# Kernel tuning notes

Hardware: AMD Instinct MI355X
Metric: run time of the kernel (lower is better)

The kernel has to match this reference:

```python
import jax, jax.numpy as jnp
import numpy as np

MAX_REL = 30
N_HEADS = 8


def conv1d(x, w, b=None, groups=1):
    # x: [B, L, Cin], w: [Cout, Cin/groups, K]  (torch Conv1d layout), 'same' padding
    pad = w.shape[-1] // 2
    y = jax.lax.conv_general_dilated(
        x, w, window_strides=(1,), padding=[(pad, pad)],
        dimension_numbers=("NLC", "OIL", "NLC"), feature_group_count=groups)
    return y if b is None else y + b


def setup_inputs() -> dict:
    key = jax.random.key(0)
    ks = jax.random.split(key, 16)
    B, L, S = 8, 1024, 512          # L = 2 * S (required by Gamma.repeat(1,2,1))
    sd, vd, dm = 512, 64, 512       # spatial_dim == d_model (residual add)
    D = 3 * vd                      # rel-pos / K,V channel dim

    def n(k, shape, s):
        return (jax.random.normal(k, shape, jnp.float32) * s).astype(jnp.float32)

    return {
        "x_spatial": jax.random.normal(ks[0], (B, L, sd), jnp.float32),
        "x_velocity": jax.random.normal(ks[1], (B, S, vd), jnp.float32),
        "w_gamma": n(ks[2], (dm, vd, 1), 0.05)[:, :, 0],      # conv_gamma 1x1, no bias -> [dm, vd]
        "w3": n(ks[3], (vd, vd, 3), 0.07), "b3": jnp.zeros((vd,), jnp.float32),
        "w5": n(ks[4], (vd, vd, 5), 0.05), "b5": jnp.zeros((vd,), jnp.float32),
        "w7": n(ks[5], (vd, vd, 7), 0.04), "b7": jnp.zeros((vd,), jnp.float32),
        "rel_table": n(ks[6], (2 * MAX_REL + 1, D), 0.05),    # embedding [61, 192]
        "dw_w": n(ks[7], (D, 1, 3), 0.3), "dw_b": jnp.zeros((D,), jnp.float32),
        "wq": n(ks[8], (dm, sd), 0.03),
        "wk": n(ks[9], (dm, D), 0.05),
        "wv": n(ks[10], (dm, D), 0.05),
        "fc_w": n(ks[11], (dm, dm), 0.03), "fc_b": jnp.zeros((dm,), jnp.float32),
        "ln_g": jnp.ones((dm,), jnp.float32), "ln_b": jnp.zeros((dm,), jnp.float32),
    }


def rel_pos_enc(ms, rel_table, dw_w, dw_b):
    # Math-equivalent reduction of the torch O(B*S^2*D) op:
    # output[b,j] = mean_i where(i==j, dwconv_row_i(fused)[j], fused[b,i,j])
    #            = ms[b,j] + mean_i rel[i,j] + (diag_conv[b,j] - fused[b,j,j]) / S
    B, S, D = ms.shape
    pos = jnp.arange(S)
    idx = jnp.clip(pos[None, :] - pos[:, None], -MAX_REL, MAX_REL) + MAX_REL  # [S,S]
    mean_rel = rel_table[idx].mean(axis=0)                                    # [S,D]
    # fused[b,i,j] = ms[b,j] + rel_table[idx[i,j]]; diagonal uses idx = MAX_REL,
    # its +/-1 neighbors along j use MAX_REL -/+ ... -> rel[i,i-1]=MAX_REL-1, rel[i,i+1]=MAX_REL+1
    center = ms + rel_table[MAX_REL]                                          # fused[b,i,i]
    left = jnp.pad(ms[:, :-1] + rel_table[MAX_REL - 1], ((0, 0), (1, 0), (0, 0)))   # conv zero-pads at i=0
    right = jnp.pad(ms[:, 1:] + rel_table[MAX_REL + 1], ((0, 0), (0, 1), (0, 0)))   # conv zero-pads at i=S-1
    diag_conv = dw_w[:, 0, 0] * left + dw_w[:, 0, 1] * center + dw_w[:, 0, 2] * right + dw_b
    return ms + mean_rel[None] + (diag_conv - center) / S


def reference(x_spatial, x_velocity, w_gamma, w3, b3, w5, b5, w7, b7,
              rel_table, dw_w, dw_b, wq, wk, wv, fc_w, fc_b, ln_g, ln_b):
    B, S, vd = x_velocity.shape
    _, L, _ = x_spatial.shape
    dm = wq.shape[0]
    dk = dm // N_HEADS

    gamma = jax.nn.sigmoid(jnp.einsum("bsc,dc->bsd", x_velocity, w_gamma))   # [B,S,dm]

    ms = jnp.concatenate([conv1d(x_velocity, w3, b3),
                          conv1d(x_velocity, w5, b5),
                          conv1d(x_velocity, w7, b7)], axis=-1)              # [B,S,3vd]
    x_pe = rel_pos_enc(ms, rel_table, dw_w, dw_b)                            # [B,S,3vd]

    q = jnp.einsum("blc,dc->bld", x_spatial, wq).reshape(B, L, N_HEADS, dk).transpose(0, 2, 1, 3)
    k = jnp.einsum("bsc,dc->bsd", x_pe, wk).reshape(B, S, N_HEADS, dk).transpose(0, 2, 1, 3)
    v = jnp.einsum("bsc,dc->bsd", x_pe, wv).reshape(B, S, N_HEADS, dk).transpose(0, 2, 1, 3)

    scores = jnp.einsum("bhld,bhsd->bhls", q, k) / jnp.sqrt(jnp.float32(dk))
    attn = jax.nn.softmax(scores, axis=-1)                                   # dropout: eval mode (identity)
    out = jnp.einsum("bhls,bhsd->bhld", attn, v)                             # [B,H,L,dk]
    out = out.transpose(0, 2, 1, 3).reshape(B, L, dm)
    out = out @ fc_w.T + fc_b

    out = jnp.tile(gamma, (1, 2, 1)) * out                                   # L == 2*S
    res = x_spatial + out
    mu = res.mean(-1, keepdims=True)
    var = res.var(-1, keepdims=True)
    return (res - mu) / jnp.sqrt(var + 1e-5) * ln_g + ln_b
```

## Files before the change

### kernel.cpp

```cpp
#include <hip/hip_runtime.h>
#include <hip/hip_bf16.h>

constexpr int B  = 8;
constexpr int L  = 1024;
constexpr int S  = 512;
constexpr int VD = 64;
constexpr int DM = 512;
constexpr int D3 = 192;
constexpr int H  = 8;
constexpr int DK = 64;

typedef __attribute__((ext_vector_type(8))) short s8v;
typedef __attribute__((ext_vector_type(4))) float f4v;

__device__ inline unsigned short f2b(float f) {
    unsigned int u = __builtin_bit_cast(unsigned int, f);
    u += 0x7fffu + ((u >> 16) & 1u);
    return (unsigned short)(u >> 16);
}
__device__ inline float b2f(unsigned int lo16) {
    return __builtin_bit_cast(float, lo16 << 16);
}

__device__ __forceinline__ void gload16(const void* g, void* l) {
    __builtin_amdgcn_global_load_lds(
        (const __attribute__((address_space(1))) void*)g,
        (__attribute__((address_space(3))) void*)l, 16, 0, 0);
}

struct CastArgs {
    const float* src[7];
    unsigned short* dst[7];
    int n[7];
    float scale[7];
};

__global__ __launch_bounds__(256) void prep_cast_k(
    CastArgs a,
    const float* __restrict__ w3, const float* __restrict__ w5,
    const float* __restrict__ w7, const float* __restrict__ dw_w,
    const float* __restrict__ rel_table, const float* __restrict__ b3,
    const float* __restrict__ b5, const float* __restrict__ b7,
    const float* __restrict__ dw_b,
    unsigned short* __restrict__ WpeT, unsigned short* __restrict__ Cp)
{
    int t = threadIdx.x;
    int y = blockIdx.y;

    if (y < 7) {
        const float* s = a.src[y];
        unsigned short* d = a.dst[y];
        int n = a.n[y];
        float sc = a.scale[y];
        for (long i = (long)(blockIdx.x * 256 + t) * 4; i < n;
             i += (long)gridDim.x * 1024) {
            float4 f = *(const float4*)(s + i);
            ushort4 o;
            o.x = f2b(f.x * sc); o.y = f2b(f.y * sc);
            o.z = f2b(f.z * sc); o.w = f2b(f.w * sc);
            *(ushort4*)(d + i) = o;
        }
        return;
    }

    if (t >= 192) return;
    int o = t;
    float inv = 1.0f / S;

    if (blockIdx.x < 640) {
        int n = blockIdx.x;
        if (n >= 576) { WpeT[n * D3 + o] = 0; return; }
        int j = n >> 6, c = n & 63, delta = j - 4;
        const float* w; int KW, P, oo;
        if (o < 64)       { w = w3; KW = 3; P = 1; oo = o; }
        else if (o < 128) { w = w5; KW = 5; P = 2; oo = o - 64; }
        else              { w = w7; KW = 7; P = 3; oo = o - 128; }
        float mu0 = dw_w[o * 3 + 0] * inv;
        float mu1 = 1.f + (dw_w[o * 3 + 1] - 1.f) * inv;
        float mu2 = dw_w[o * 3 + 2] * inv;
        float acc = 0.f;
        int k;
        k = delta + 1 + P; if (k >= 0 && k < KW) acc += mu0 * w[(oo * 64 + c) * KW + k];
        k = delta + P;     if (k >= 0 && k < KW) acc += mu1 * w[(oo * 64 + c) * KW + k];
        k = delta - 1 + P; if (k >= 0 && k < KW) acc += mu2 * w[(oo * 64 + c) * KW + k];
        WpeT[n * D3 + o] = f2b(acc);
        return;
    }

    int j = blockIdx.x - 640;
    float acc = 0.f;
#pragma unroll
    for (int r = 1; r < 60; r++) {
        int i = j - (r - 30);
        if (i >= 0 && i < S) acc += rel_table[r * D3 + o];
    }
    float c60 = (float)max(0, j - 29);
    float c0  = (float)max(0, (S - 30) - j);
    acc += c60 * rel_table[60 * D3 + o] + c0 * rel_table[0 * D3 + o];
    float mean_rel = acc * inv;

    float bo  = (o < 64) ? b3[o] : (o < 128) ? b5[o - 64] : b7[o - 128];
    float dw0 = dw_w[o * 3], dw1 = dw_w[o * 3 + 1], dw2 = dw_w[o * 3 + 2];
    float r29 = rel_table[29 * D3 + o], r30 = rel_table[30 * D3 + o],
          r31 = rel_table[31 * D3 + o];
    float alpha = 1.f + (dw1 - 1.f) * inv, beta = dw0 * inv, gamma = dw2 * inv;

    float cp = mean_rel + bo * alpha + (dw1 * r30 + dw_b[o] - r30) * inv;
    if (j > 0)     cp += beta * bo + dw0 * r29 * inv;
    if (j < S - 1) cp += gamma * bo + dw2 * r31 * inv;
    Cp[j * D3 + o] = f2b(cp);
}

__global__ __launch_bounds__(256) void pre_gemm5_k(
    const unsigned short* __restrict__ wk_bf,
    const unsigned short* __restrict__ wv_bf,
    const unsigned short* __restrict__ WpeT,
    const unsigned short* __restrict__ Cp,
    const unsigned short* __restrict__ xv_bf,
    const unsigned short* __restrict__ wg_bf,
    unsigned short* __restrict__ WEff,
    unsigned short* __restrict__ Cb,
    unsigned short* __restrict__ gamma_bf)
{
    int z = blockIdx.z, mx = blockIdx.x, ny = blockIdx.y;
    const unsigned short *A, *Bm;
    unsigned short* C;
    int K, lda, ldb, ldc;
    if (z < 2) {
        if (mx >= 4) return;
        A = z ? wv_bf : wk_bf; Bm = WpeT; C = WEff + (long)z * DM * 640;
        K = D3; lda = D3; ldb = D3; ldc = 640;
    } else if (z < 4) {
        if (mx >= 4 || ny >= 4) return;
        A = Cp; Bm = (z == 2) ? wk_bf : wv_bf; C = Cb + (long)(z - 2) * S * DM;
        K = D3; lda = D3; ldb = D3; ldc = DM;
    } else {
        if (ny >= 4) return;
        A = xv_bf; Bm = wg_bf; C = gamma_bf;
        K = VD; lda = VD; ldb = VD; ldc = DM;
    }

    __shared__ __align__(16) unsigned short As[128 * 64];
    __shared__ __align__(16) unsigned short Bs[128 * 64];

    int t = threadIdx.x;
    int l = t & 63, w = t >> 6;
    int lx = l & 15, lh = l >> 4;
    int wr = w >> 1, wc = w & 1;
    int m0 = mx * 128, n0 = ny * 128;

    f4v acc[4][4] = {};

    for (int k0 = 0; k0 < K; k0 += 64) {
        __syncthreads();
#pragma unroll
        for (int p = 0; p < 4; p++) {
            int flat = p * 256 + t;
            int r = flat >> 3, c = flat & 7;
            int csw = (c ^ (r & 7)) * 8;
            gload16(A  + (long)(m0 + r) * lda + k0 + csw, As + flat * 8);
            gload16(Bm + (long)(n0 + r) * ldb + k0 + csw, Bs + flat * 8);
        }
        __syncthreads();
#pragma unroll
        for (int ks = 0; ks < 2; ks++) {
            s8v af[4], bf[4];
#pragma unroll
            for (int i = 0; i < 4; i++) {
                int ra = wr * 64 + i * 16 + lx;
                af[i] = *(const s8v*)(As + ra * 64 + (((ks * 4 + lh) ^ (ra & 7)) * 8));
                int rb = wc * 64 + i * 16 + lx;
                bf[i] = *(const s8v*)(Bs + rb * 64 + (((ks * 4 + lh) ^ (rb & 7)) * 8));
            }
#pragma unroll
            for (int i = 0; i < 4; i++)
#pragma unroll
                for (int j = 0; j < 4; j++)
                    acc[i][j] = __builtin_amdgcn_mfma_f32_16x16x32_bf16(
                        af[i], bf[j], acc[i][j], 0, 0, 0);
        }
    }

#pragma unroll
    for (int i = 0; i < 4; i++) {
#pragma unroll
        for (int r = 0; r < 4; r++) {
            int m = m0 + wr * 64 + i * 16 + lh * 4 + r;
#pragma unroll
            for (int j = 0; j < 4; j++) {
                int n = n0 + wc * 64 + j * 16 + lx;
                C[(long)m * ldc + n] = f2b(acc[i][j][r]);
            }
        }
    }
}

__global__ __launch_bounds__(256) void qconv_k(
    const unsigned short* __restrict__ xs_bf,
    const unsigned short* __restrict__ wq_bf,
    unsigned short* __restrict__ qbuf,
    const unsigned short* __restrict__ xvb,
    const unsigned short* __restrict__ Weff0,
    const unsigned short* __restrict__ bias0,
    unsigned short* __restrict__ Cout0,
    const unsigned short* __restrict__ zsrc)
{
    __shared__ __align__(16) unsigned short As[128 * 64];
    __shared__ __align__(16) unsigned short Bs[128 * 64];

    int zt = blockIdx.z;
    int t = threadIdx.x;
    int l = t & 63, w = t >> 6;
    int lx = l & 15, lh = l >> 4;
    int wr = w >> 1, wc = w & 1;

    f4v acc[4][4] = {};

    if (zt == 0) {
        int m0 = blockIdx.x * 128, n0 = blockIdx.y * 128;
        for (int k0 = 0; k0 < DM; k0 += 64) {
            __syncthreads();
#pragma unroll
            for (int p = 0; p < 4; p++) {
                int flat = p * 256 + t;
                int r = flat >> 3, c = flat & 7;
                int csw = (c ^ (r & 7)) * 8;
                gload16(xs_bf + (long)(m0 + r) * DM + k0 + csw, As + flat * 8);
                gload16(wq_bf + (long)(n0 + r) * DM + k0 + csw, Bs + flat * 8);
            }
            __syncthreads();
#pragma unroll
            for (int ks = 0; ks < 2; ks++) {
                s8v af[4], bf[4];
#pragma unroll
                for (int i = 0; i < 4; i++) {
                    int ra = wr * 64 + i * 16 + lx;
                    af[i] = *(const s8v*)(As + ra * 64 + (((ks * 4 + lh) ^ (ra & 7)) * 8));
                    int rb = wc * 64 + i * 16 + lx;
                    bf[i] = *(const s8v*)(Bs + rb * 64 + (((ks * 4 + lh) ^ (rb & 7)) * 8));
                }
#pragma unroll
                for (int i = 0; i < 4; i++)
#pragma unroll
                    for (int j = 0; j < 4; j++)
                        acc[i][j] = __builtin_amdgcn_mfma_f32_16x16x32_bf16(
                            af[i], bf[j], acc[i][j], 0, 0, 0);
            }
        }
#pragma unroll
        for (int i = 0; i < 4; i++) {
#pragma unroll
            for (int r = 0; r < 4; r++) {
                int m = m0 + wr * 64 + i * 16 + lh * 4 + r;
#pragma unroll
                for (int j = 0; j < 4; j++) {
                    int n = n0 + wc * 64 + j * 16 + lx;
                    qbuf[(long)m * DM + n] = f2b(acc[i][j][r]);
                }
            }
        }
        return;
    }

    if (blockIdx.x >= 32) return;
    int z = zt - 1;
    const unsigned short* Weff = Weff0 + (long)z * DM * 640;
    const unsigned short* bias2d = bias0 + (long)z * S * DM;
    unsigned short* Cout = Cout0 + (long)z * B * S * DM;

    int m0 = blockIdx.x * 128, n0 = blockIdx.y * 128;
    int b = m0 >> 9, s0 = m0 & 511;

    for (int j = 0; j < 9; j++) {
        __syncthreads();
#pragma unroll
        for (int p = 0; p < 4; p++) {
            int flat = p * 256 + t;
            int r = flat >> 3, c = flat & 7;
            int csw = (c ^ (r & 7)) * 8;
            int ss = s0 + r + j - 4;
            const unsigned short* asrc = (ss >= 0 && ss < S)
                ? xvb + ((long)b * S + ss) * VD + csw : zsrc;
            gload16(asrc, As + flat * 8);
            gload16(Weff + (long)(n0 + r) * 640 + j * 64 + csw, Bs + flat * 8);
        }
        __syncthreads();
#pragma unroll
        for (int ks = 0; ks < 2; ks++) {
            s8v af[4], bf[4];
#pragma unroll
            for (int i = 0; i < 4; i++) {
                int ra = wr * 64 + i * 16 + lx;
                af[i] = *(const s8v*)(As + ra * 64 + (((ks * 4 + lh) ^ (ra & 7)) * 8));
                int rb = wc * 64 + i * 16 + lx;
                bf[i] = *(const s8v*)(Bs + rb * 64 + (((ks * 4 + lh) ^ (rb & 7)) * 8));
            }
#pragma unroll
            for (int i = 0; i < 4; i++)
#pragma unroll
                for (int jj = 0; jj < 4; jj++)
                    acc[i][jj] = __builtin_amdgcn_mfma_f32_16x16x32_bf16(
                        af[i], bf[jj], acc[i][jj], 0, 0, 0);
        }
    }

#pragma unroll
    for (int i = 0; i < 4; i++) {
#pragma unroll
        for (int r = 0; r < 4; r++) {
            int m = m0 + wr * 64 + i * 16 + lh * 4 + r;
            int s = m & 511;
#pragma unroll
            for (int jj = 0; jj < 4; jj++) {
                int n = n0 + wc * 64 + jj * 16 + lx;
                Cout[(long)m * DM + n] =
                    f2b(acc[i][jj][r] + b2f(bias2d[(long)s * DM + n]));
            }
        }
    }
}

__global__ __launch_bounds__(256) void gemm_fc_k(
    const unsigned short* __restrict__ A, const unsigned short* __restrict__ Bm,
    unsigned short* __restrict__ Cout, const float* __restrict__ bias)
{
    __shared__ __align__(16) unsigned short As[128 * 64];
    __shared__ __align__(16) unsigned short Bs[128 * 64];

    int t = threadIdx.x;
    int l = t & 63, w = t >> 6;
    int lx = l & 15, lh = l >> 4;
    int wr = w >> 1, wc = w & 1;
    int m0 = blockIdx.x * 128, n0 = blockIdx.y * 128;

    f4v acc[4][4] = {};

    for (int k0 = 0; k0 < DM; k0 += 64) {
        __syncthreads();
#pragma unroll
        for (int p = 0; p < 4; p++) {
            int flat = p * 256 + t;
            int r = flat >> 3, c = flat & 7;
            int csw = (c ^ (r & 7)) * 8;
            gload16(A  + (long)(m0 + r) * DM + k0 + csw, As + flat * 8);
            gload16(Bm + (long)(n0 + r) * DM + k0 + csw, Bs + flat * 8);
        }
        __syncthreads();
#pragma unroll
        for (int ks = 0; ks < 2; ks++) {
            s8v af[4], bf[4];
#pragma unroll
            for (int i = 0; i < 4; i++) {
                int ra = wr * 64 + i * 16 + lx;
                af[i] = *(const s8v*)(As + ra * 64 + (((ks * 4 + lh) ^ (ra & 7)) * 8));
                int rb = wc * 64 + i * 16 + lx;
                bf[i] = *(const s8v*)(Bs + rb * 64 + (((ks * 4 + lh) ^ (rb & 7)) * 8));
            }
#pragma unroll
            for (int i = 0; i < 4; i++)
#pragma unroll
                for (int j = 0; j < 4; j++)
                    acc[i][j] = __builtin_amdgcn_mfma_f32_16x16x32_bf16(
                        af[i], bf[j], acc[i][j], 0, 0, 0);
        }
    }

#pragma unroll
    for (int i = 0; i < 4; i++) {
#pragma unroll
        for (int r = 0; r < 4; r++) {
            int m = m0 + wr * 64 + i * 16 + lh * 4 + r;
#pragma unroll
            for (int j = 0; j < 4; j++) {
                int n = n0 + wc * 64 + j * 16 + lx;
                Cout[(long)m * DM + n] = f2b(acc[i][j][r] + bias[n]);
            }
        }
    }
}

__global__ __launch_bounds__(256) void attn_mfma_k(
    const unsigned short* __restrict__ qb, const unsigned short* __restrict__ kb,
    const unsigned short* __restrict__ vb, unsigned short* __restrict__ ob)
{
    __shared__ __align__(16) unsigned short Qs[64 * 64];
    __shared__ __align__(16) unsigned short Ks[64 * 64];
    __shared__ __align__(16) unsigned short Vt[64 * 64];
    __shared__ __align__(16) unsigned short Ps[64 * 64];

    int lt = blockIdx.x, h = blockIdx.y, b = blockIdx.z;
    int t = threadIdx.x, l = t & 63, w = t >> 6, lx = l & 15, lh = l >> 4;

    const unsigned short* qg = qb + ((long)(b * L + lt * 64)) * DM + h * 64;
    const unsigned short* kg = kb + ((long)b * S) * DM + h * 64;
    const unsigned short* vg = vb + ((long)b * S) * DM + h * 64;

#pragma unroll
    for (int p = 0; p < 2; p++) {
        int flat = p * 256 + t;
        int r = flat >> 3, c = flat & 7;
        s8v v = *(const s8v*)(qg + (long)r * DM + c * 8);
        *(s8v*)(Qs + r * 64 + ((c ^ (r & 7)) * 8)) = v;
    }

    int kr0 = t >> 3, kc = t & 7;
    int vs = t & 63, vdq = t >> 6;
    s8v k0, k1, v0, v1;

    auto loadKV = [&](int st) {
        k0 = *(const s8v*)(kg + (long)(st * 64 + kr0) * DM + kc * 8);
        k1 = *(const s8v*)(kg + (long)(st * 64 + 32 + kr0) * DM + kc * 8);
        const unsigned short* vp = vg + (long)(st * 64 + vs) * DM + vdq * 16;
        v0 = *(const s8v*)(vp);
        v1 = *(const s8v*)(vp + 8);
    };
    auto writeKV = [&]() {
        *(s8v*)(Ks + kr0 * 64 + ((kc ^ (kr0 & 7)) * 8)) = k0;
        int r2 = 32 + kr0;
        *(s8v*)(Ks + r2 * 64 + ((kc ^ (r2 & 7)) * 8)) = k1;
#pragma unroll
        for (int e = 0; e < 8; e++) {
            int d1 = vdq * 16 + e;
            Vt[d1 * 64 + (((vs >> 3) ^ (d1 & 7)) * 8) + (vs & 7)] =
                (unsigned short)v0[e];
            int d2 = vdq * 16 + 8 + e;
            Vt[d2 * 64 + (((vs >> 3) ^ (d2 & 7)) * 8) + (vs & 7)] =
                (unsigned short)v1[e];
        }
    };

    loadKV(0);
    writeKV();
    __syncthreads();

    float lrow[4] = {0.f, 0.f, 0.f, 0.f};
    f4v oacc[4] = {};

    for (int st = 0; st < S / 64; st++) {
        if (st < S / 64 - 1) loadKV(st + 1);

        f4v pacc[4] = {};
        __builtin_amdgcn_s_setprio(1);
#pragma unroll
        for (int ks = 0; ks < 2; ks++) {
            int qr = w * 16 + lx;
            s8v a = *(const s8v*)(Qs + qr * 64 + (((ks * 4 + lh) ^ (qr & 7)) * 8));
#pragma unroll
            for (int jf = 0; jf < 4; jf++) {
                int kr = jf * 16 + lx;
                s8v bf = *(const s8v*)(Ks + kr * 64 + (((ks * 4 + lh) ^ (kr & 7)) * 8));
                pacc[jf] = __builtin_amdgcn_mfma_f32_16x16x32_bf16(a, bf, pacc[jf], 0, 0, 0);
            }
        }
        __builtin_amdgcn_s_setprio(0);

#pragma unroll
        for (int r = 0; r < 4; r++) {
            int prow = w * 16 + lh * 4 + r;
#pragma unroll
            for (int jf = 0; jf < 4; jf++) {
                float pe = __builtin_amdgcn_exp2f(pacc[jf][r]);
                lrow[r] += pe;
                int col = jf * 16 + lx;
                Ps[prow * 64 + (((col >> 3) ^ (prow & 7)) * 8) + (col & 7)] = f2b(pe);
            }
        }
        asm volatile("s_waitcnt lgkmcnt(0)" ::: "memory");

        __builtin_amdgcn_s_setprio(1);
#pragma unroll
        for (int ks2 = 0; ks2 < 2; ks2++) {
            int pr = w * 16 + lx;
            s8v pa = *(const s8v*)(Ps + pr * 64 + (((ks2 * 4 + lh) ^ (pr & 7)) * 8));
#pragma unroll
            for (int df = 0; df < 4; df++) {
                int vr = df * 16 + lx;
                s8v vf = *(const s8v*)(Vt + vr * 64 + (((ks2 * 4 + lh) ^ (vr & 7)) * 8));
                oacc[df] = __builtin_amdgcn_mfma_f32_16x16x32_bf16(pa, vf, oacc[df], 0, 0, 0);
            }
        }
        __builtin_amdgcn_s_setprio(0);
        __syncthreads();
        if (st < S / 64 - 1) {
            writeKV();
            __syncthreads();
        }
    }

    unsigned short* og = ob + ((long)(b * L + lt * 64 + w * 16)) * DM + h * 64;
#pragma unroll
    for (int r = 0; r < 4; r++) {
        float ls = lrow[r];
#pragma unroll
        for (int msk = 1; msk < 16; msk <<= 1) ls += __shfl_xor(ls, msk);
        float inv = 1.f / ls;
#pragma unroll
        for (int df = 0; df < 4; df++)
            og[(long)(lh * 4 + r) * DM + df * 16 + lx] = f2b(oacc[df][r] * inv);
    }
}

__global__ __launch_bounds__(256) void final_k(
    const float* __restrict__ xs, const unsigned short* __restrict__ fcb,
    const unsigned short* __restrict__ gb,
    const float* __restrict__ ln_g, const float* __restrict__ ln_b,
    float* __restrict__ out)
{
    int bl = blockIdx.x;
    int b = bl >> 10, lq = bl & 1023;
    int t = threadIdx.x;
    int d0 = t * 2;
    const unsigned short* g = gb + ((long)b * S + (lq & 511)) * DM;

    __shared__ float red[2][4];

    float2 xv = *(const float2*)(xs + (long)bl * DM + d0);
    unsigned int fp = *(const unsigned int*)(fcb + (long)bl * DM + d0);
    unsigned int gp = *(const unsigned int*)(g + d0);

    float fo0 = b2f(fp & 0xffffu), fo1 = b2f(fp >> 16);
    float ga0 = 1.f / (1.f + __expf(-b2f(gp & 0xffffu)));
    float ga1 = 1.f / (1.f + __expf(-b2f(gp >> 16)));
    float r0 = xv.x + ga0 * fo0;
    float r1 = xv.y + ga1 * fo1;

    float sum = r0 + r1, sumsq = r0 * r0 + r1 * r1;
#pragma unroll
    for (int msk = 1; msk < 64; msk <<= 1) {
        sum   += __shfl_xor(sum, msk);
        sumsq += __shfl_xor(sumsq, msk);
    }
    int wave = t >> 6;
    if ((t & 63) == 0) { red[0][wave] = sum; red[1][wave] = sumsq; }
    __syncthreads();
    float tot   = red[0][0] + red[0][1] + red[0][2] + red[0][3];
    float totsq = red[1][0] + red[1][1] + red[1][2] + red[1][3];

    float mu  = tot * (1.0f / DM);
    float var = totsq * (1.0f / DM) - mu * mu;
    float inv = rsqrtf(var + 1e-5f);

    float2 lg = *(const float2*)(ln_g + d0);
    float2 lb = *(const float2*)(ln_b + d0);
    float2 o;
    o.x = (r0 - mu) * inv * lg.x + lb.x;
    o.y = (r1 - mu) * inv * lg.y + lb.y;
    *(float2*)(out + (long)bl * DM + d0) = o;
}

extern "C" void kernel_launch(void* const* d_in, const int* in_sizes, int n_in,
                              void* d_out, int out_size, void* d_ws, size_t ws_size,
                              hipStream_t stream) {
    (void)in_sizes; (void)n_in; (void)out_size; (void)ws_size;

    const float* x_spatial  = (const float*)d_in[0];
    const float* x_velocity = (const float*)d_in[1];
    const float* w_gamma    = (const float*)d_in[2];
    const float* w3 = (const float*)d_in[3];
    const float* b3 = (const float*)d_in[4];
    const float* w5 = (const float*)d_in[5];
    const float* b5 = (const float*)d_in[6];
    const float* w7 = (const float*)d_in[7];
    const float* b7 = (const float*)d_in[8];
    const float* rel_table = (const float*)d_in[9];
    const float* dw_w = (const float*)d_in[10];
    const float* dw_b = (const float*)d_in[11];
    const float* wq   = (const float*)d_in[12];
    const float* wk   = (const float*)d_in[13];
    const float* wv   = (const float*)d_in[14];
    const float* fc_w = (const float*)d_in[15];
    const float* fc_b = (const float*)d_in[16];
    const float* ln_g = (const float*)d_in[17];
    const float* ln_b = (const float*)d_in[18];
    float* out = (float*)d_out;

    char* p = (char*)d_ws;
    auto alloc = [&](size_t bytes) {
        char* r = p;
        p += (bytes + 255) & ~(size_t)255;
        return r;
    };
    unsigned short* gamma_bf = (unsigned short*)alloc((size_t)B * S * DM * 2);
    unsigned short* fcb      = (unsigned short*)alloc((size_t)B * L * DM * 2);
    unsigned short* xs_bf   = (unsigned short*)alloc((size_t)B * L * DM * 2);
    unsigned short* xv_bf   = (unsigned short*)alloc((size_t)B * S * VD * 2);
    unsigned short* qbuf    = (unsigned short*)alloc((size_t)B * L * DM * 2);
    unsigned short* kbuf    = (unsigned short*)alloc((size_t)B * S * DM * 2);
    unsigned short* vbuf    = (unsigned short*)alloc((size_t)B * S * DM * 2);
    unsigned short* attn_bf = (unsigned short*)alloc((size_t)B * L * DM * 2);
    unsigned short* wq_bf   = (unsigned short*)alloc((size_t)DM * DM * 2);
    unsigned short* wk_bf   = (unsigned short*)alloc((size_t)DM * D3 * 2);
    unsigned short* wv_bf   = (unsigned short*)alloc((size_t)DM * D3 * 2);
    unsigned short* fcw_bf  = (unsigned short*)alloc((size_t)DM * DM * 2);
    unsigned short* wg_bf   = (unsigned short*)alloc((size_t)DM * VD * 2);
    unsigned short* WpeT    = (unsigned short*)alloc((size_t)640 * D3 * 2);
    unsigned short* Cp      = (unsigned short*)alloc((size_t)S * D3 * 2);
    unsigned short* WkEff   = (unsigned short*)alloc((size_t)DM * 640 * 2);
    unsigned short* WvEff   = (unsigned short*)alloc((size_t)DM * 640 * 2);
    unsigned short* Ckb     = (unsigned short*)alloc((size_t)S * DM * 2);
    unsigned short* Cvb     = (unsigned short*)alloc((size_t)S * DM * 2);
    (void)wv_bf; (void)WvEff; (void)Cvb;

    CastArgs ca;
    ca.src[0] = x_spatial;  ca.dst[0] = xs_bf;  ca.n[0] = B * L * DM; ca.scale[0] = 1.f;
    ca.src[1] = x_velocity; ca.dst[1] = xv_bf;  ca.n[1] = B * S * VD; ca.scale[1] = 1.f;
    ca.src[2] = wq;         ca.dst[2] = wq_bf;  ca.n[2] = DM * DM;    ca.scale[2] = 0.125f * 1.44269504089f;
    ca.src[3] = wk;         ca.dst[3] = wk_bf;  ca.n[3] = DM * D3;    ca.scale[3] = 1.f;
    ca.src[4] = wv;         ca.dst[4] = wv_bf;  ca.n[4] = DM * D3;    ca.scale[4] = 1.f;
    ca.src[5] = fc_w;       ca.dst[5] = fcw_bf; ca.n[5] = DM * DM;    ca.scale[5] = 1.f;
    ca.src[6] = w_gamma;    ca.dst[6] = wg_bf;  ca.n[6] = DM * VD;    ca.scale[6] = 1.f;
    prep_cast_k<<<dim3(1152, 8), 256, 0, stream>>>(
        ca, w3, w5, w7, dw_w, rel_table, b3, b5, b7, dw_b, WpeT, Cp);

    pre_gemm5_k<<<dim3(32, 5, 5), 256, 0, stream>>>(
        wk_bf, wv_bf, WpeT, Cp, xv_bf, wg_bf, WkEff, Ckb, gamma_bf);

    qconv_k<<<dim3(64, 4, 3), 256, 0, stream>>>(
        xs_bf, wq_bf, qbuf, xv_bf, WkEff, Ckb, kbuf,
        WkEff + 576 );

    attn_mfma_k<<<dim3(L / 64, H, B), 256, 0, stream>>>(qbuf, kbuf, vbuf, attn_bf);

    gemm_fc_k<<<dim3(64, 4), 256, 0, stream>>>(attn_bf, fcw_bf, fcb, fc_b);

    final_k<<<dim3(B * L), 256, 0, stream>>>(
        x_spatial, fcb, gamma_bf, ln_g, ln_b, out);
}
```

Baseline: 188.9 us.

## Double attention query tile, use 128x64 GEMM tiles, merge K/V buffers

The attention kernel now handles 128 query rows per block instead of 64, so each K/V tile staged in LDS is reused across twice as many queries. The Q projection and fc GEMMs move to a 128x64 output tile to double block count. Shared GEMM bodies are factored out, and the K and V buffers are placed contiguously. The larger attention tile raises register and LDS use and halves grid size, which may reduce occupancy.

```diff
diff --git a/kernel.cpp b/kernel.cpp
--- a/kernel.cpp
+++ b/kernel.cpp
@@ -8,7 +8,6 @@
 constexpr int DM = 512;
 constexpr int D3 = 192;
 constexpr int H  = 8;
-constexpr int DK = 64;
 
 typedef __attribute__((ext_vector_type(8))) short s8v;
 typedef __attribute__((ext_vector_type(4))) float f4v;
@@ -34,6 +33,191 @@
     int n[7];
     float scale[7];
 };
+
+__device__ __forceinline__ void gemm128_body(
+    const unsigned short* __restrict__ A, const unsigned short* __restrict__ Bm,
+    unsigned short* __restrict__ C, const float* __restrict__ bias,
+    int K, int lda, int ldb, int ldc, int m0, int n0,
+    unsigned short* As, unsigned short* Bs, int t)
+{
+    int l = t & 63, w = t >> 6;
+    int lx = l & 15, lh = l >> 4;
+    int wr = w >> 1, wc = w & 1;
+
+    f4v acc[4][4] = {};
+
+    for (int k0 = 0; k0 < K; k0 += 64) {
+        __syncthreads();
+#pragma unroll
+        for (int p = 0; p < 4; p++) {
+            int flat = p * 256 + t;
+            int r = flat >> 3, c = flat & 7;
+            int csw = (c ^ (r & 7)) * 8;
+            gload16(A  + (long)(m0 + r) * lda + k0 + csw, As + flat * 8);
+            gload16(Bm + (long)(n0 + r) * ldb + k0 + csw, Bs + flat * 8);
+        }
+        __syncthreads();
+#pragma unroll
+        for (int ks = 0; ks < 2; ks++) {
+            s8v af[4], bf[4];
+#pragma unroll
+            for (int i = 0; i < 4; i++) {
+                int ra = wr * 64 + i * 16 + lx;
+                af[i] = *(const s8v*)(As + ra * 64 + (((ks * 4 + lh) ^ (ra & 7)) * 8));
+                int rb = wc * 64 + i * 16 + lx;
+                bf[i] = *(const s8v*)(Bs + rb * 64 + (((ks * 4 + lh) ^ (rb & 7)) * 8));
+            }
+#pragma unroll
+            for (int i = 0; i < 4; i++)
+#pragma unroll
+                for (int j = 0; j < 4; j++)
+                    acc[i][j] = __builtin_amdgcn_mfma_f32_16x16x32_bf16(
+                        af[i], bf[j], acc[i][j], 0, 0, 0);
+        }
+    }
+
+#pragma unroll
+    for (int i = 0; i < 4; i++) {
+#pragma unroll
+        for (int r = 0; r < 4; r++) {
+            int m = m0 + wr * 64 + i * 16 + lh * 4 + r;
+#pragma unroll
+            for (int j = 0; j < 4; j++) {
+                int n = n0 + wc * 64 + j * 16 + lx;
+                float v = acc[i][j][r];
+                if (bias) v += bias[n];
+                C[(long)m * ldc + n] = f2b(v);
+            }
+        }
+    }
+}
+
+__device__ __forceinline__ void gemm_mn64_body(
+    const unsigned short* __restrict__ A, const unsigned short* __restrict__ Bm,
+    unsigned short* __restrict__ C, const float* __restrict__ bias,
+    int K, int m0, int n0, unsigned short* As, unsigned short* Bs, int t)
+{
+    int l = t & 63, w = t >> 6;
+    int lx = l & 15, lh = l >> 4;
+
+    f4v acc[2][4] = {};
+
+    for (int k0 = 0; k0 < K; k0 += 64) {
+        __syncthreads();
+#pragma unroll
+        for (int p = 0; p < 4; p++) {
+            int flat = p * 256 + t;
+            int r = flat >> 3, c = flat & 7;
+            int csw = (c ^ (r & 7)) * 8;
+            gload16(A + (long)(m0 + r) * DM + k0 + csw, As + flat * 8);
+        }
+#pragma unroll
+        for (int p = 0; p < 2; p++) {
+            int flat = p * 256 + t;
+            int r = flat >> 3, c = flat & 7;
+            int csw = (c ^ (r & 7)) * 8;
+            gload16(Bm + (long)(n0 + r) * DM + k0 + csw, Bs + flat * 8);
+        }
+        __syncthreads();
+#pragma unroll
+        for (int ks = 0; ks < 2; ks++) {
+            s8v af[2], bf[4];
+#pragma unroll
+            for (int i = 0; i < 2; i++) {
+                int ra = w * 32 + i * 16 + lx;
+                af[i] = *(const s8v*)(As + ra * 64 + (((ks * 4 + lh) ^ (ra & 7)) * 8));
+            }
+#pragma unroll
+            for (int j = 0; j < 4; j++) {
+                int rb = j * 16 + lx;
+                bf[j] = *(const s8v*)(Bs + rb * 64 + (((ks * 4 + lh) ^ (rb & 7)) * 8));
+            }
+#pragma unroll
+            for (int i = 0; i < 2; i++)
+#pragma unroll
+                for (int j = 0; j < 4; j++)
+                    acc[i][j] = __builtin_amdgcn_mfma_f32_16x16x32_bf16(
+                        af[i], bf[j], acc[i][j], 0, 0, 0);
+        }
+    }
+
+#pragma unroll
+    for (int i = 0; i < 2; i++) {
+#pragma unroll
+        for (int r = 0; r < 4; r++) {
+            int m = m0 + w * 32 + i * 16 + lh * 4 + r;
+#pragma unroll
+            for (int j = 0; j < 4; j++) {
+                int n = n0 + j * 16 + lx;
+                float v = acc[i][j][r];
+                if (bias) v += bias[n];
+                C[(long)m * DM + n] = f2b(v);
+            }
+        }
+    }
+}
+
+__device__ __forceinline__ void conv_body(
+    const unsigned short* __restrict__ xvb, const unsigned short* __restrict__ Weff,
+    const unsigned short* __restrict__ bias2d, unsigned short* __restrict__ Cout,
+    const unsigned short* __restrict__ zsrc, int m0, int n0,
+    unsigned short* As, unsigned short* Bs, int t)
+{
+    int l = t & 63, w = t >> 6;
+    int lx = l & 15, lh = l >> 4;
+    int wr = w >> 1, wc = w & 1;
+    int b = m0 >> 9, s0 = m0 & 511;
+
+    f4v acc[4][4] = {};
+
+    for (int j = 0; j < 9; j++) {
+        __syncthreads();
+#pragma unroll
+        for (int p = 0; p < 4; p++) {
+            int flat = p * 256 + t;
+            int r = flat >> 3, c = flat & 7;
+            int csw = (c ^ (r & 7)) * 8;
+            int ss = s0 + r + j - 4;
+            const unsigned short* asrc = (ss >= 0 && ss < S)
+                ? xvb + ((long)b * S + ss) * VD + csw : zsrc;
+            gload16(asrc, As + flat * 8);
+            gload16(Weff + (long)(n0 + r) * 640 + j * 64 + csw, Bs + flat * 8);
+        }
+        __syncthreads();
+#pragma unroll
+        for (int ks = 0; ks < 2; ks++) {
+            s8v af[4], bf[4];
+#pragma unroll
+            for (int i = 0; i < 4; i++) {
+                int ra = wr * 64 + i * 16 + lx;
+                af[i] = *(const s8v*)(As + ra * 64 + (((ks * 4 + lh) ^ (ra & 7)) * 8));
+                int rb = wc * 64 + i * 16 + lx;
+                bf[i] = *(const s8v*)(Bs + rb * 64 + (((ks * 4 + lh) ^ (rb & 7)) * 8));
+            }
+#pragma unroll
+            for (int i = 0; i < 4; i++)
+#pragma unroll
+                for (int jj = 0; jj < 4; jj++)
+                    acc[i][jj] = __builtin_amdgcn_mfma_f32_16x16x32_bf16(
+                        af[i], bf[jj], acc[i][jj], 0, 0, 0);
+        }
+    }
+
+#pragma unroll
+    for (int i = 0; i < 4; i++) {
+#pragma unroll
+        for (int r = 0; r < 4; r++) {
+            int m = m0 + wr * 64 + i * 16 + lh * 4 + r;
+            int s = m & 511;
+#pragma unroll
+            for (int jj = 0; jj < 4; jj++) {
+                int n = n0 + wc * 64 + jj * 16 + lx;
+                Cout[(long)m * DM + n] =
+                    f2b(acc[i][jj][r] + b2f(bias2d[(long)s * DM + n]));
+            }
+        }
+    }
+}
 
 __global__ __launch_bounds__(256) void prep_cast_k(
     CastArgs a,
@@ -142,57 +326,8 @@
 
     __shared__ __align__(16) unsigned short As[128 * 64];
     __shared__ __align__(16) unsigned short Bs[128 * 64];
-
-    int t = threadIdx.x;
-    int l = t & 63, w = t >> 6;
-    int lx = l & 15, lh = l >> 4;
-    int wr = w >> 1, wc = w & 1;
-    int m0 = mx * 128, n0 = ny * 128;
-
-    f4v acc[4][4] = {};
-
-    for (int k0 = 0; k0 < K; k0 += 64) {
-        __syncthreads();
-#pragma unroll
-        for (int p = 0; p < 4; p++) {
-            int flat = p * 256 + t;
-            int r = flat >> 3, c = flat & 7;
-            int csw = (c ^ (r & 7)) * 8;
-            gload16(A  + (long)(m0 + r) * lda + k0 + csw, As + flat * 8);
-            gload16(Bm + (long)(n0 + r) * ldb + k0 + csw, Bs + flat * 8);
-        }
-        __syncthreads();
-#pragma unroll
-        for (int ks = 0; ks < 2; ks++) {
-            s8v af[4], bf[4];
-#pragma unroll
-            for (int i = 0; i < 4; i++) {
-                int ra = wr * 64 + i * 16 + lx;
-                af[i] = *(const s8v*)(As + ra * 64 + (((ks * 4 + lh) ^ (ra & 7)) * 8));
-                int rb = wc * 64 + i * 16 + lx;
-                bf[i] = *(const s8v*)(Bs + rb * 64 + (((ks * 4 + lh) ^ (rb & 7)) * 8));
-            }
-#pragma unroll
-            for (int i = 0; i < 4; i++)
-#pragma unroll
-                for (int j = 0; j < 4; j++)
-                    acc[i][j] = __builtin_amdgcn_mfma_f32_16x16x32_bf16(
-                        af[i], bf[j], acc[i][j], 0, 0, 0);
-        }
-    }
-
-#pragma unroll
-    for (int i = 0; i < 4; i++) {
-#pragma unroll
-        for (int r = 0; r < 4; r++) {
-            int m = m0 + wr * 64 + i * 16 + lh * 4 + r;
-#pragma unroll
-            for (int j = 0; j < 4; j++) {
-                int n = n0 + wc * 64 + j * 16 + lx;
-                C[(long)m * ldc + n] = f2b(acc[i][j][r]);
-            }
-        }
-    }
+    gemm128_body(A, Bm, C, nullptr, K, lda, ldb, ldc,
+                 mx * 128, ny * 128, As, Bs, threadIdx.x);
 }
 
 __global__ __launch_bounds__(256) void qconv_k(
@@ -207,197 +342,39 @@
 {
     __shared__ __align__(16) unsigned short As[128 * 64];
     __shared__ __align__(16) unsigned short Bs[128 * 64];
-
-    int zt = blockIdx.z;
-    int t = threadIdx.x;
-    int l = t & 63, w = t >> 6;
-    int lx = l & 15, lh = l >> 4;
-    int wr = w >> 1, wc = w & 1;
-
-    f4v acc[4][4] = {};
+    int zt = blockIdx.z, t = threadIdx.x;
 
     if (zt == 0) {
-        int m0 = blockIdx.x * 128, n0 = blockIdx.y * 128;
-        for (int k0 = 0; k0 < DM; k0 += 64) {
-            __syncthreads();
-#pragma unroll
-            for (int p = 0; p < 4; p++) {
-                int flat = p * 256 + t;
-                int r = flat >> 3, c = flat & 7;
-                int csw = (c ^ (r & 7)) * 8;
-                gload16(xs_bf + (long)(m0 + r) * DM + k0 + csw, As + flat * 8);
-                gload16(wq_bf + (long)(n0 + r) * DM + k0 + csw, Bs + flat * 8);
-            }
-            __syncthreads();
-#pragma unroll
-            for (int ks = 0; ks < 2; ks++) {
-                s8v af[4], bf[4];
-#pragma unroll
-                for (int i = 0; i < 4; i++) {
-                    int ra = wr * 64 + i * 16 + lx;
-                    af[i] = *(const s8v*)(As + ra * 64 + (((ks * 4 + lh) ^ (ra & 7)) * 8));
-                    int rb = wc * 64 + i * 16 + lx;
-                    bf[i] = *(const s8v*)(Bs + rb * 64 + (((ks * 4 + lh) ^ (rb & 7)) * 8));
-                }
-#pragma unroll
-                for (int i = 0; i < 4; i++)
-#pragma unroll
-                    for (int j = 0; j < 4; j++)
-                        acc[i][j] = __builtin_amdgcn_mfma_f32_16x16x32_bf16(
-                            af[i], bf[j], acc[i][j], 0, 0, 0);
-            }
-        }
-#pragma unroll
-        for (int i = 0; i < 4; i++) {
-#pragma unroll
-            for (int r = 0; r < 4; r++) {
-                int m = m0 + wr * 64 + i * 16 + lh * 4 + r;
-#pragma unroll
-                for (int j = 0; j < 4; j++) {
-                    int n = n0 + wc * 64 + j * 16 + lx;
-                    qbuf[(long)m * DM + n] = f2b(acc[i][j][r]);
-                }
-            }
-        }
+        gemm_mn64_body(xs_bf, wq_bf, qbuf, nullptr, DM,
+                       blockIdx.x * 128, blockIdx.y * 64, As, Bs, t);
         return;
     }
-
-    if (blockIdx.x >= 32) return;
+    if (blockIdx.x >= 32 || blockIdx.y >= 4) return;
     int z = zt - 1;
-    const unsigned short* Weff = Weff0 + (long)z * DM * 640;
-    const unsigned short* bias2d = bias0 + (long)z * S * DM;
-    unsigned short* Cout = Cout0 + (long)z * B * S * DM;
-
-    int m0 = blockIdx.x * 128, n0 = blockIdx.y * 128;
-    int b = m0 >> 9, s0 = m0 & 511;
-
-    for (int j = 0; j < 9; j++) {
-        __syncthreads();
-#pragma unroll
-        for (int p = 0; p < 4; p++) {
-            int flat = p * 256 + t;
-            int r = flat >> 3, c = flat & 7;
-            int csw = (c ^ (r & 7)) * 8;
-            int ss = s0 + r + j - 4;
-            const unsigned short* asrc = (ss >= 0 && ss < S)
-                ? xvb + ((long)b * S + ss) * VD + csw : zsrc;
-            gload16(asrc, As + flat * 8);
-            gload16(Weff + (long)(n0 + r) * 640 + j * 64 + csw, Bs + flat * 8);
-        }
-        __syncthreads();
-#pragma unroll
-        for (int ks = 0; ks < 2; ks++) {
-            s8v af[4], bf[4];
-#pragma unroll
-            for (int i = 0; i < 4; i++) {
-                int ra = wr * 64 + i * 16 + lx;
-                af[i] = *(const s8v*)(As + ra * 64 + (((ks * 4 + lh) ^ (ra & 7)) * 8));
-                int rb = wc * 64 + i * 16 + lx;
-                bf[i] = *(const s8v*)(Bs + rb * 64 + (((ks * 4 + lh) ^ (rb & 7)) * 8));
-            }
-#pragma unroll
-            for (int i = 0; i < 4; i++)
-#pragma unroll
-                for (int jj = 0; jj < 4; jj++)
-                    acc[i][jj] = __builtin_amdgcn_mfma_f32_16x16x32_bf16(
-                        af[i], bf[jj], acc[i][jj], 0, 0, 0);
-        }
-    }
-
-#pragma unroll
-    for (int i = 0; i < 4; i++) {
-#pragma unroll
-        for (int r = 0; r < 4; r++) {
-            int m = m0 + wr * 64 + i * 16 + lh * 4 + r;
-            int s = m & 511;
-#pragma unroll
-            for (int jj = 0; jj < 4; jj++) {
-                int n = n0 + wc * 64 + jj * 16 + lx;
-                Cout[(long)m * DM + n] =
-                    f2b(acc[i][jj][r] + b2f(bias2d[(long)s * DM + n]));
-            }
-        }
-    }
-}
-
-__global__ __launch_bounds__(256) void gemm_fc_k(
-    const unsigned short* __restrict__ A, const unsigned short* __restrict__ Bm,
-    unsigned short* __restrict__ Cout, const float* __restrict__ bias)
-{
-    __shared__ __align__(16) unsigned short As[128 * 64];
-    __shared__ __align__(16) unsigned short Bs[128 * 64];
-
-    int t = threadIdx.x;
-    int l = t & 63, w = t >> 6;
-    int lx = l & 15, lh = l >> 4;
-    int wr = w >> 1, wc = w & 1;
-    int m0 = blockIdx.x * 128, n0 = blockIdx.y * 128;
-
-    f4v acc[4][4] = {};
-
-    for (int k0 = 0; k0 < DM; k0 += 64) {
-        __syncthreads();
-#pragma unroll
-        for (int p = 0; p < 4; p++) {
-            int flat = p * 256 + t;
-            int r = flat >> 3, c = flat & 7;
-            int csw = (c ^ (r & 7)) * 8;
-            gload16(A  + (long)(m0 + r) * DM + k0 + csw, As + flat * 8);
-            gload16(Bm + (long)(n0 + r) * DM + k0 + csw, Bs + flat * 8);
-        }
-        __syncthreads();
-#pragma unroll
-        for (int ks = 0; ks < 2; ks++) {
-            s8v af[4], bf[4];
-#pragma unroll
-            for (int i = 0; i < 4; i++) {
-                int ra = wr * 64 + i * 16 + lx;
-                af[i] = *(const s8v*)(As + ra * 64 + (((ks * 4 + lh) ^ (ra & 7)) * 8));
-                int rb = wc * 64 + i * 16 + lx;
-                bf[i] = *(const s8v*)(Bs + rb * 64 + (((ks * 4 + lh) ^ (rb & 7)) * 8));
-            }
-#pragma unroll
-            for (int i = 0; i < 4; i++)
-#pragma unroll
-                for (int j = 0; j < 4; j++)
-                    acc[i][j] = __builtin_amdgcn_mfma_f32_16x16x32_bf16(
-                        af[i], bf[j], acc[i][j], 0, 0, 0);
-        }
-    }
-
-#pragma unroll
-    for (int i = 0; i < 4; i++) {
-#pragma unroll
-        for (int r = 0; r < 4; r++) {
-            int m = m0 + wr * 64 + i * 16 + lh * 4 + r;
-#pragma unroll
-            for (int j = 0; j < 4; j++) {
-                int n = n0 + wc * 64 + j * 16 + lx;
-                Cout[(long)m * DM + n] = f2b(acc[i][j][r] + bias[n]);
-            }
-        }
-    }
+    conv_body(xvb, Weff0 + (long)z * DM * 640, bias0 + (long)z * S * DM,
+              Cout0 + (long)z * B * S * DM, zsrc,
+              blockIdx.x * 128, blockIdx.y * 128, As, Bs, t);
 }
 
 __global__ __launch_bounds__(256) void attn_mfma_k(
     const unsigned short* __restrict__ qb, const unsigned short* __restrict__ kb,
     const unsigned short* __restrict__ vb, unsigned short* __restrict__ ob)
 {
-    __shared__ __align__(16) unsigned short Qs[64 * 64];
+    __shared__ __align__(16) unsigned short Qs[128 * 64];
     __shared__ __align__(16) unsigned short Ks[64 * 64];
     __shared__ __align__(16) unsigned short Vt[64 * 64];
-    __shared__ __align__(16) unsigned short Ps[64 * 64];
+    __shared__ __align__(16) unsigned short Ps[128 * 64];
 
     int lt = blockIdx.x, h = blockIdx.y, b = blockIdx.z;
     int t = threadIdx.x, l = t & 63, w = t >> 6, lx = l & 15, lh = l >> 4;
 
-    const unsigned short* qg = qb + ((long)(b * L + lt * 64)) * DM + h * 64;
+    const unsigned short* qg = qb + ((long)(b * L + lt * 128)) * DM + h * 64;
     const unsigned short* kg = kb + ((long)b * S) * DM + h * 64;
     const unsigned short* vg = vb + ((long)b * S) * DM + h * 64;
 
 #pragma unroll
-    for (int p = 0; p < 2; p++) {
-        int flat = p * 256 + t;
+    for (int pp = 0; pp < 4; pp++) {
+        int flat = pp * 256 + t;
         int r = flat >> 3, c = flat & 7;
         s8v v = *(const s8v*)(qg + (long)r * DM + c * 8);
         *(s8v*)(Qs + r * 64 + ((c ^ (r & 7)) * 8)) = v;
@@ -421,11 +398,9 @@
 #pragma unroll
         for (int e = 0; e < 8; e++) {
             int d1 = vdq * 16 + e;
-            Vt[d1 * 64 + (((vs >> 3) ^ (d1 & 7)) * 8) + (vs & 7)] =
-                (unsigned short)v0[e];
+            Vt[d1 * 64 + (((vs >> 3) ^ (d1 & 7)) * 8) + (vs & 7)] = (unsigned short)v0[e];
             int d2 = vdq * 16 + 8 + e;
-            Vt[d2 * 64 + (((vs >> 3) ^ (d2 & 7)) * 8) + (vs & 7)] =
-                (unsigned short)v1[e];
+            Vt[d2 * 64 + (((vs >> 3) ^ (d2 & 7)) * 8) + (vs & 7)] = (unsigned short)v1[e];
         }
     };
 
@@ -433,34 +408,39 @@
     writeKV();
     __syncthreads();
 
-    float lrow[4] = {0.f, 0.f, 0.f, 0.f};
-    f4v oacc[4] = {};
+    float lrow[2][4] = {};
+    f4v oacc[2][4] = {};
 
     for (int st = 0; st < S / 64; st++) {
         if (st < S / 64 - 1) loadKV(st + 1);
 
-        f4v pacc[4] = {};
+        f4v pacc[2][4] = {};
         __builtin_amdgcn_s_setprio(1);
 #pragma unroll
+        for (int sub = 0; sub < 2; sub++)
+#pragma unroll
         for (int ks = 0; ks < 2; ks++) {
-            int qr = w * 16 + lx;
+            int qr = sub * 64 + w * 16 + lx;
             s8v a = *(const s8v*)(Qs + qr * 64 + (((ks * 4 + lh) ^ (qr & 7)) * 8));
 #pragma unroll
             for (int jf = 0; jf < 4; jf++) {
                 int kr = jf * 16 + lx;
                 s8v bf = *(const s8v*)(Ks + kr * 64 + (((ks * 4 + lh) ^ (kr & 7)) * 8));
-                pacc[jf] = __builtin_amdgcn_mfma_f32_16x16x32_bf16(a, bf, pacc[jf], 0, 0, 0);
+                pacc[sub][jf] = __builtin_amdgcn_mfma_f32_16x16x32_bf16(
+                    a, bf, pacc[sub][jf], 0, 0, 0);
             }
         }
         __builtin_amdgcn_s_setprio(0);
 
 #pragma unroll
+        for (int sub = 0; sub < 2; sub++)
+#pragma unroll
         for (int r = 0; r < 4; r++) {
-            int prow = w * 16 + lh * 4 + r;
+            int prow = sub * 64 + w * 16 + lh * 4 + r;
 #pragma unroll
             for (int jf = 0; jf < 4; jf++) {
-                float pe = __builtin_amdgcn_exp2f(pacc[jf][r]);
-                lrow[r] += pe;
+                float pe = __builtin_amdgcn_exp2f(pacc[sub][jf][r]);
+                lrow[sub][r] += pe;
                 int col = jf * 16 + lx;
                 Ps[prow * 64 + (((col >> 3) ^ (prow & 7)) * 8) + (col & 7)] = f2b(pe);
             }
@@ -469,14 +449,17 @@
 
         __builtin_amdgcn_s_setprio(1);
 #pragma unroll
+        for (int sub = 0; sub < 2; sub++)
+#pragma unroll
         for (int ks2 = 0; ks2 < 2; ks2++) {
-            int pr = w * 16 + lx;
+            int pr = sub * 64 + w * 16 + lx;
             s8v pa = *(const s8v*)(Ps + pr * 64 + (((ks2 * 4 + lh) ^ (pr & 7)) * 8));
 #pragma unroll
             for (int df = 0; df < 4; df++) {
                 int vr = df * 16 + lx;
                 s8v vf = *(const s8v*)(Vt + vr * 64 + (((ks2 * 4 + lh) ^ (vr & 7)) * 8));
-                oacc[df] = __builtin_amdgcn_mfma_f32_16x16x32_bf16(pa, vf, oacc[df], 0, 0, 0);
+                oacc[sub][df] = __builtin_amdgcn_mfma_f32_16x16x32_bf16(
+                    pa, vf, oacc[sub][df], 0, 0, 0);
             }
         }
         __builtin_amdgcn_s_setprio(0);
@@ -487,17 +470,32 @@
         }
     }
 
-    unsigned short* og = ob + ((long)(b * L + lt * 64 + w * 16)) * DM + h * 64;
-#pragma unroll
-    for (int r = 0; r < 4; r++) {
-        float ls = lrow[r];
-#pragma unroll
-        for (int msk = 1; msk < 16; msk <<= 1) ls += __shfl_xor(ls, msk);
-        float inv = 1.f / ls;
-#pragma unroll
-        for (int df = 0; df < 4; df++)
-            og[(long)(lh * 4 + r) * DM + df * 16 + lx] = f2b(oacc[df][r] * inv);
-    }
+#pragma unroll
+    for (int sub = 0; sub < 2; sub++) {
+        unsigned short* og = ob +
+            ((long)(b * L + lt * 128 + sub * 64 + w * 16)) * DM + h * 64;
+#pragma unroll
+        for (int r = 0; r < 4; r++) {
+            float ls = lrow[sub][r];
+#pragma unroll
+            for (int msk = 1; msk < 16; msk <<= 1) ls += __shfl_xor(ls, msk);
+            float invl = 1.f / ls;
+#pragma unroll
+            for (int df = 0; df < 4; df++)
+                og[(long)(lh * 4 + r) * DM + df * 16 + lx] =
+                    f2b(oacc[sub][df][r] * invl);
+        }
+    }
+}
+
+__global__ __launch_bounds__(256) void gemm_fc_k(
+    const unsigned short* __restrict__ A, const unsigned short* __restrict__ Bm,
+    unsigned short* __restrict__ Cout, const float* __restrict__ bias)
+{
+    __shared__ __align__(16) unsigned short As[128 * 64];
+    __shared__ __align__(16) unsigned short Bs[128 * 64];
+    gemm_mn64_body(A, Bm, Cout, bias, DM,
+                   blockIdx.x * 128, blockIdx.y * 64, As, Bs, threadIdx.x);
 }
 
 __global__ __launch_bounds__(256) void final_k(
@@ -514,15 +512,15 @@
 
     __shared__ float red[2][4];
 
-    float2 xv = *(const float2*)(xs + (long)bl * DM + d0);
+    float2 xv2 = *(const float2*)(xs + (long)bl * DM + d0);
     unsigned int fp = *(const unsigned int*)(fcb + (long)bl * DM + d0);
     unsigned int gp = *(const unsigned int*)(g + d0);
 
     float fo0 = b2f(fp & 0xffffu), fo1 = b2f(fp >> 16);
     float ga0 = 1.f / (1.f + __expf(-b2f(gp & 0xffffu)));
     float ga1 = 1.f / (1.f + __expf(-b2f(gp >> 16)));
-    float r0 = xv.x + ga0 * fo0;
-    float r1 = xv.y + ga1 * fo1;
+    float r0 = xv2.x + ga0 * fo0;
+    float r1 = xv2.y + ga1 * fo1;
 
     float sum = r0 + r1, sumsq = r0 * r0 + r1 * r1;
 #pragma unroll
@@ -574,10 +572,10 @@
     const float* ln_b = (const float*)d_in[18];
     float* out = (float*)d_out;
 
-    char* p = (char*)d_ws;
+    char* pw = (char*)d_ws;
     auto alloc = [&](size_t bytes) {
-        char* r = p;
-        p += (bytes + 255) & ~(size_t)255;
+        char* r = pw;
+        pw += (bytes + 255) & ~(size_t)255;
         return r;
     };
     unsigned short* gamma_bf = (unsigned short*)alloc((size_t)B * S * DM * 2);
@@ -585,8 +583,7 @@
     unsigned short* xs_bf   = (unsigned short*)alloc((size_t)B * L * DM * 2);
     unsigned short* xv_bf   = (unsigned short*)alloc((size_t)B * S * VD * 2);
     unsigned short* qbuf    = (unsigned short*)alloc((size_t)B * L * DM * 2);
-    unsigned short* kbuf    = (unsigned short*)alloc((size_t)B * S * DM * 2);
-    unsigned short* vbuf    = (unsigned short*)alloc((size_t)B * S * DM * 2);
+    unsigned short* kvbuf   = (unsigned short*)alloc((size_t)2 * B * S * DM * 2);
     unsigned short* attn_bf = (unsigned short*)alloc((size_t)B * L * DM * 2);
     unsigned short* wq_bf   = (unsigned short*)alloc((size_t)DM * DM * 2);
     unsigned short* wk_bf   = (unsigned short*)alloc((size_t)DM * D3 * 2);
@@ -595,11 +592,8 @@
     unsigned short* wg_bf   = (unsigned short*)alloc((size_t)DM * VD * 2);
     unsigned short* WpeT    = (unsigned short*)alloc((size_t)640 * D3 * 2);
     unsigned short* Cp      = (unsigned short*)alloc((size_t)S * D3 * 2);
-    unsigned short* WkEff   = (unsigned short*)alloc((size_t)DM * 640 * 2);
-    unsigned short* WvEff   = (unsigned short*)alloc((size_t)DM * 640 * 2);
-    unsigned short* Ckb     = (unsigned short*)alloc((size_t)S * DM * 2);
-    unsigned short* Cvb     = (unsigned short*)alloc((size_t)S * DM * 2);
-    (void)wv_bf; (void)WvEff; (void)Cvb;
+    unsigned short* WkEff   = (unsigned short*)alloc((size_t)2 * DM * 640 * 2);
+    unsigned short* Ckb     = (unsigned short*)alloc((size_t)2 * S * DM * 2);
 
     CastArgs ca;
     ca.src[0] = x_spatial;  ca.dst[0] = xs_bf;  ca.n[0] = B * L * DM; ca.scale[0] = 1.f;
@@ -615,13 +609,13 @@
     pre_gemm5_k<<<dim3(32, 5, 5), 256, 0, stream>>>(
         wk_bf, wv_bf, WpeT, Cp, xv_bf, wg_bf, WkEff, Ckb, gamma_bf);
 
-    qconv_k<<<dim3(64, 4, 3), 256, 0, stream>>>(
-        xs_bf, wq_bf, qbuf, xv_bf, WkEff, Ckb, kbuf,
-        WkEff + 576 );
-
-    attn_mfma_k<<<dim3(L / 64, H, B), 256, 0, stream>>>(qbuf, kbuf, vbuf, attn_bf);
-
-    gemm_fc_k<<<dim3(64, 4), 256, 0, stream>>>(attn_bf, fcw_bf, fcb, fc_b);
+    qconv_k<<<dim3(64, 8, 3), 256, 0, stream>>>(
+        xs_bf, wq_bf, qbuf, xv_bf, WkEff, Ckb, kvbuf, WkEff + 576);
+
+    attn_mfma_k<<<dim3(L / 128, H, B), 256, 0, stream>>>(
+        qbuf, kvbuf, kvbuf + (long)B * S * DM, attn_bf);
+
+    gemm_fc_k<<<dim3(64, 8), 256, 0, stream>>>(attn_bf, fcw_bf, fcb, fc_b);
 
     final_k<<<dim3(B * L), 256, 0, stream>>>(
         x_spatial, fcb, gamma_bf, ln_g, ln_b, out);
```

Measured after the change: 192.1 us. About the same (+1.7%).
